# Kernel tuning notes

Measured on AMD Instinct MI355X. Metric: run time of the kernel, lower is better.

## Reference

```python
import jax, jax.numpy as jnp
import numpy as np

TEMPERATURE = 8.0  # sqrt(d_k=64)
NEG = -1e15


def setup_inputs() -> dict:
    key = jax.random.key(0)
    k1, k2, k3, k4, k5 = jax.random.split(key, 5)
    BH, L, D = 64, 1024, 64  # B=4 examples x H=16 heads
    B = 4
    q = jax.random.normal(k1, (BH, L, D), dtype=jnp.float32)
    k = jax.random.normal(k2, (BH, L, D), dtype=jnp.float32)
    v = jax.random.normal(k3, (BH, L, D), dtype=jnp.float32)
    mask = jax.random.randint(k4, (BH, L, L), 0, 2).astype(jnp.bool_)
    edge = jax.random.randint(k5, (B, L, L), 0, 2).astype(jnp.int32)
    return {"q": q, "k": k, "v": v, "mask": mask, "edge": edge}


def reference(q, k, v, mask, edge):
    # attn = q @ k^T / temperature : [BH, L, L]
    attn = jnp.einsum('bld,bmd->blm', q, k) / TEMPERATURE
    # edge.repeat(BH // B, 1, 1): torch repeat == tile along batch dim
    rep = attn.shape[0] // edge.shape[0]
    edge_t = jnp.tile(edge, (rep, 1, 1))
    attn = jnp.where(edge_t == 0, NEG, attn)
    attn = jnp.where(mask, NEG, attn)
    attn = jax.nn.softmax(attn, axis=2)
    # dropout p=0 -> identity
    output = jnp.einsum('blm,bmd->bld', attn, v)
    return (output, attn)
```

## Files before the change

kernel.cpp:

```cpp
#include <hip/hip_runtime.h>
#include <hip/hip_bf16.h>

#define L_ 1024
#define BH_ 64
#define NEGV (-1e15f)
#define QSCALE 0.18033688011112043f

typedef float f32x4 __attribute__((ext_vector_type(4)));
typedef short s16x8 __attribute__((ext_vector_type(8)));
typedef unsigned short ushort_t;

__device__ __forceinline__ unsigned short f2bf(float f) {
    return __builtin_bit_cast(unsigned short, __float2bfloat16(f));
}
__device__ __forceinline__ unsigned selw(uint4 v, int i) {
    switch (i) { case 0: return v.x; case 1: return v.y; case 2: return v.z; default: return v.w; }
}
__device__ __forceinline__ unsigned spread4(unsigned n) {
    return (n & 1u) | ((n & 2u) << 3) | ((n & 4u) << 6) | ((n & 8u) << 9);
}
__device__ __forceinline__ unsigned pack_bytes_nz(uint4 m) {
    unsigned u = 0;
    #pragma unroll
    for (int k = 0; k < 4; ++k) {
        const unsigned x = selw(m, k);
        u |= ((x & 0x000000FFu) ? 1u : 0u) << (k * 4 + 0);
        u |= ((x & 0x0000FF00u) ? 1u : 0u) << (k * 4 + 1);
        u |= ((x & 0x00FF0000u) ? 1u : 0u) << (k * 4 + 2);
        u |= ((x & 0xFF000000u) ? 1u : 0u) << (k * 4 + 3);
    }
    return u;
}

template<bool TESTZERO>
__device__ __forceinline__ unsigned row_bits_i32(uint4 e0, uint4 e1, uint4 e2, uint4 e3, int ln)
{
    #define BAL_(v) (TESTZERO ? __ballot((v) == 0u) : __ballot((v) != 0u))
    const unsigned long long b00 = BAL_(e0.x), b01 = BAL_(e0.y), b02 = BAL_(e0.z), b03 = BAL_(e0.w);
    const unsigned long long b10 = BAL_(e1.x), b11 = BAL_(e1.y), b12 = BAL_(e1.z), b13 = BAL_(e1.w);
    const unsigned long long b20 = BAL_(e2.x), b21 = BAL_(e2.y), b22 = BAL_(e2.z), b23 = BAL_(e2.w);
    const unsigned long long b30 = BAL_(e3.x), b31 = BAL_(e3.y), b32 = BAL_(e3.z), b33 = BAL_(e3.w);
    #undef BAL_
    const int q0 = ln >> 4, sh = (ln & 15) << 2;
    unsigned u = 0;
    unsigned long long bp;
    bp = q0 == 0 ? b00 : q0 == 1 ? b10 : q0 == 2 ? b20 : b30;
    u |= spread4((unsigned)((bp >> sh) & 0xF)) << 0;
    bp = q0 == 0 ? b01 : q0 == 1 ? b11 : q0 == 2 ? b21 : b31;
    u |= spread4((unsigned)((bp >> sh) & 0xF)) << 1;
    bp = q0 == 0 ? b02 : q0 == 1 ? b12 : q0 == 2 ? b22 : b32;
    u |= spread4((unsigned)((bp >> sh) & 0xF)) << 2;
    bp = q0 == 0 ? b03 : q0 == 1 ? b13 : q0 == 2 ? b23 : b33;
    u |= spread4((unsigned)((bp >> sh) & 0xF)) << 3;
    return u;
}

__global__ __launch_bounds__(256)
void prep1(const int* __restrict__ edgep, ushort_t* __restrict__ mb)
{
    const int wv = threadIdx.x >> 6, ln = threadIdx.x & 63;
    #pragma unroll
    for (int it = 0; it < 4; ++it) {
        const int r   = (blockIdx.x << 4) + (it << 2) + wv;
        const int eb  = r >> 10, row = r & 1023;
        const int rb  = ((eb << 10) + row) << 10;
        const uint4 e0 = *((const uint4*)(edgep + rb) + ln);
        const uint4 e1 = *((const uint4*)(edgep + rb + 256) + ln);
        const uint4 e2 = *((const uint4*)(edgep + rb + 512) + ln);
        const uint4 e3 = *((const uint4*)(edgep + rb + 768) + ln);
        const unsigned u = row_bits_i32<true>(e0, e1, e2, e3, ln);
        const int pp = ((ln & 7) << 3) + (ln >> 3);
        #pragma unroll
        for (int bq = 0; bq < 16; ++bq) {
            const int bh = (bq << 2) + eb;
            mb[((size_t)((bh << 10) + row) << 6) + pp] = (ushort_t)u;
        }
    }
}

__global__ __launch_bounds__(256)
void prep2(const float* __restrict__ vp, const unsigned char* __restrict__ maskp,
           ushort_t* __restrict__ mb, ushort_t* __restrict__ vt)
{
    __shared__ float tile[64][68];
    const int b = blockIdx.x;
    if (b < 2048) {
        const int wv = threadIdx.x >> 6, ln = threadIdx.x & 63;
        unsigned det = 0;
        const unsigned* mu = (const unsigned*)maskp;
        #pragma unroll
        for (int i = 0; i < 16; ++i) det |= mu[i];
        const bool mask_i32 = ((det & 0xFFFFFF00u) == 0u);
        #pragma unroll
        for (int it = 0; it < 8; ++it) {
            const int r = (b << 5) + (it << 2) + wv;
            unsigned u;
            if (!mask_i32) {
                const uint4 m = *((const uint4*)(maskp + ((size_t)r << 10)) + ln);
                u = pack_bytes_nz(m);
            } else {
                const int* mp = (const int*)maskp + ((size_t)r << 10);
                const uint4 m0 = *((const uint4*)mp + ln);
                const uint4 m1 = *((const uint4*)(mp + 256) + ln);
                const uint4 m2 = *((const uint4*)(mp + 512) + ln);
                const uint4 m3 = *((const uint4*)(mp + 768) + ln);
                u = row_bits_i32<false>(m0, m1, m2, m3, ln);
            }
            const int pp = ((ln & 7) << 3) + (ln >> 3);
            mb[((size_t)r << 6) + pp] |= (ushort_t)u;
        }
    } else {
        const int idx = b - 2048;
        const int bh = idx >> 2, kq = (idx & 3) << 8;
        const int t = threadIdx.x;
        for (int ks = 0; ks < 4; ++ks) {
            const int k0 = kq + (ks << 6);
            {
                const int kr = t >> 2, d0 = (t & 3) << 4;
                const float* src = vp + ((size_t)(((bh << 10) + k0 + kr)) << 6) + d0;
                const float4 v0 = *(const float4*)(src);
                const float4 v1 = *(const float4*)(src + 4);
                const float4 v2 = *(const float4*)(src + 8);
                const float4 v3 = *(const float4*)(src + 12);
                *(float4*)&tile[kr][d0]      = v0;
                *(float4*)&tile[kr][d0 + 4]  = v1;
                *(float4*)&tile[kr][d0 + 8]  = v2;
                *(float4*)&tile[kr][d0 + 12] = v3;
            }
            __syncthreads();
            {
                const int d = t >> 2, kc = (t & 3) << 4;
                unsigned uu[8];
                #pragma unroll
                for (int j = 0; j < 16; ++j) {
                    const unsigned short h = f2bf(tile[kc + j][d]);
                    if (j & 1) uu[j >> 1] |= ((unsigned)h) << 16;
                    else       uu[j >> 1] = (unsigned)h;
                }
                ushort_t* dst = vt + ((size_t)((bh << 6) + d) << 10) + k0 + kc;
                *(uint4*)(dst)     = (uint4){uu[0], uu[1], uu[2], uu[3]};
                *(uint4*)(dst + 8) = (uint4){uu[4], uu[5], uu[6], uu[7]};
            }
            __syncthreads();
        }
    }
}

__device__ __forceinline__ void kwrite(ushort_t* stg, int tid, float4 r0, float4 r1, float4 r2, float4 r3)
{
    s16x8 w0, w1;
    w0[0] = (short)f2bf(r0.x); w0[1] = (short)f2bf(r0.y);
    w0[2] = (short)f2bf(r0.z); w0[3] = (short)f2bf(r0.w);
    w0[4] = (short)f2bf(r1.x); w0[5] = (short)f2bf(r1.y);
    w0[6] = (short)f2bf(r1.z); w0[7] = (short)f2bf(r1.w);
    w1[0] = (short)f2bf(r2.x); w1[1] = (short)f2bf(r2.y);
    w1[2] = (short)f2bf(r2.z); w1[3] = (short)f2bf(r2.w);
    w1[4] = (short)f2bf(r3.x); w1[5] = (short)f2bf(r3.y);
    w1[6] = (short)f2bf(r3.z); w1[7] = (short)f2bf(r3.w);
    char* base = (char*)stg + ((tid >> 2) << 7);
    const int sw = (tid >> 2) & 7;
    const int j0 = (tid & 3) << 1;
    *(s16x8*)(base + ((j0 ^ sw) << 4)) = w0;
    *(s16x8*)(base + (((j0 + 1) ^ sw) << 4)) = w1;
}

template<int USE_WS>
__global__ __launch_bounds__(512, 6)
void attn_main(const float* __restrict__ qp, const float* __restrict__ kp,
               const float* __restrict__ vp, const unsigned char* __restrict__ maskp,
               const int* __restrict__ edgep, float* __restrict__ outO,
               float* __restrict__ outA, const ushort_t* __restrict__ vtp,
               const ushort_t* __restrict__ mbp)
{
    __shared__ __align__(16) ushort_t p_lds[16 * 1024];
    __shared__ __align__(16) ushort_t stage[8192];
    __shared__ __align__(16) ushort_t q_lds[1024];
    __shared__ float part[16][8];
    __shared__ float gred[16];

    const int tid  = threadIdx.x;
    const int lane = tid & 63;
    const int w    = tid >> 6;
    const int g    = lane >> 4;
    const int ln   = lane & 15;

    const int bid  = blockIdx.x;
    const int xcd  = bid & 7;
    const int slot = bid >> 3;
    const int bh   = xcd + ((slot >> 6) << 3);
    const int r0   = (slot & 63) << 4;

    bool mask_i32 = false;
    if (!USE_WS) {
        unsigned det = 0;
        const unsigned* mu = (const unsigned*)maskp;
        #pragma unroll
        for (int i = 0; i < 16; ++i) det |= mu[i];
        mask_i32 = ((det & 0xFFFFFF00u) == 0u);
    }

    uint4 br[4];
    if (USE_WS) {
        const ushort_t* mrow = mbp + ((size_t)(((bh << 10) + r0 + (g << 2))) << 6) + (w << 3);
        br[0] = *(const uint4*)(mrow);
        br[1] = *(const uint4*)(mrow + 64);
        br[2] = *(const uint4*)(mrow + 128);
        br[3] = *(const uint4*)(mrow + 192);
    }

    float4 k00, k01, k02, k03;
    {
        const float4* src = (const float4*)(kp + ((size_t)(bh << 10) << 6)) + (tid << 2);
        k00 = src[0]; k01 = src[1]; k02 = src[2]; k03 = src[3];
    }
    if (tid < 256) {
        const float4 qv = *((const float4*)(qp + ((size_t)((bh << 10) + r0) << 6)) + tid);
        const unsigned lo = (unsigned)f2bf(qv.x * QSCALE) | ((unsigned)f2bf(qv.y * QSCALE) << 16);
        const unsigned hi = (unsigned)f2bf(qv.z * QSCALE) | ((unsigned)f2bf(qv.w * QSCALE) << 16);
        const int qrow = tid >> 4, qch = (tid & 15) >> 1;
        char* qd = (char*)q_lds + (qrow << 7) + (((qch ^ (qrow & 7))) << 4) + ((tid & 1) << 3);
        uint2 u2; u2.x = lo; u2.y = hi;
        *(uint2*)qd = u2;
    }
    kwrite(stage, tid, k00, k01, k02, k03);
    __syncthreads();

    const int swp = ln & 7;
    const s16x8 a0 = *(const s16x8*)((char*)q_lds + (ln << 7) + ((g ^ swp) << 4));
    const s16x8 a1 = *(const s16x8*)((char*)q_lds + (ln << 7) + (((4 + g) ^ swp) << 4));

    float rs[4] = {0.f, 0.f, 0.f, 0.f};

    #pragma unroll
    for (int kt = 0; kt < 8; ++kt) {
        float4 nx0, nx1, nx2, nx3;
        uint4 vx0, vx1;
        if (kt < 7) {
            const float4* src = (const float4*)(kp + ((size_t)(((bh << 10) + ((kt + 1) << 7))) << 6)) + (tid << 2);
            nx0 = src[0]; nx1 = src[1]; nx2 = src[2]; nx3 = src[3];
        } else if (USE_WS) {
            const uint4* vs = (const uint4*)(vtp + ((size_t)((bh << 6) + (tid >> 3)) << 10) + ((tid & 7) << 4));
            vx0 = vs[0]; vx1 = vs[1];
        }

        const char* kb = (const char*)stage + (((w << 4) + ln) << 7);
        const s16x8 b0 = *(const s16x8*)(kb + ((g ^ swp) << 4));
        const s16x8 b1 = *(const s16x8*)(kb + (((4 + g) ^ swp) << 4));
        f32x4 acc = {0.f, 0.f, 0.f, 0.f};
        acc = __builtin_amdgcn_mfma_f32_16x16x32_bf16(a0, b0, acc, 0, 0, 0);
        acc = __builtin_amdgcn_mfma_f32_16x16x32_bf16(a1, b1, acc, 0, 0, 0);

        #pragma unroll
        for (int reg = 0; reg < 4; ++reg) {
            float sv = acc[reg];
            if (USE_WS) {
                const unsigned mw = selw(br[reg], kt >> 1);
                if ((mw >> (((kt & 1) << 4) + ln)) & 1u) sv = NEGV;
            } else {
                const int row = r0 + (g << 2) + reg;
                const int col = (kt << 7) + (w << 4) + ln;
                int mv;
                if (mask_i32) mv = ((const int*)maskp)[((size_t)((bh << 10) + row) << 10) + col];
                else          mv = (int)maskp[((size_t)((bh << 10) + row) << 10) + col];
                if (edgep[((size_t)((((bh & 3) << 10) + row)) << 10) + col] == 0 || mv != 0) sv = NEGV;
            }
            const float e = __builtin_amdgcn_exp2f(sv);
            rs[reg] += e;
            const int prow = (g << 2) + reg;
            char* pd = (char*)p_lds + (prow << 11)
                     + ((((kt << 4) + (w << 1) + (ln >> 3)) ^ (prow & 7)) << 4) + ((ln & 7) << 1);
            *(ushort_t*)pd = f2bf(e);
        }
        __syncthreads();
        if (kt < 7) {
            kwrite(stage, tid, nx0, nx1, nx2, nx3);
        } else if (USE_WS) {
            char* bse = (char*)stage + ((tid >> 3) << 8);
            const int sw2 = (tid >> 3) & 7;
            const int ch0 = (tid & 7) << 1;
            *(uint4*)(bse + ((ch0 ^ sw2) << 4)) = vx0;
            *(uint4*)(bse + (((ch0 + 1) ^ sw2) << 4)) = vx1;
        }
        __syncthreads();
    }

    #pragma unroll
    for (int reg = 0; reg < 4; ++reg) {
        float s = rs[reg];
        s += __shfl_xor(s, 1);
        s += __shfl_xor(s, 2);
        s += __shfl_xor(s, 4);
        s += __shfl_xor(s, 8);
        if (ln == 0) part[(g << 2) + reg][w] = s;
    }
    __syncthreads();
    if (tid < 16) {
        float s = part[tid][0];
        #pragma unroll
        for (int i = 1; i < 8; ++i) s += part[tid][i];
        gred[tid] = __builtin_amdgcn_rcpf(s);
    }
    __syncthreads();

    const int dt = w & 3, kh = w >> 2;
    f32x4 acco = {0.f, 0.f, 0.f, 0.f};
    #pragma unroll
    for (int kt = 0; kt < 8; ++kt) {
        uint4 vx0, vx1;
        if (USE_WS && kt < 7) {
            const uint4* vs = (const uint4*)(vtp + ((size_t)((bh << 6) + (tid >> 3)) << 10)
                                             + ((kt + 1) << 7) + ((tid & 7) << 4));
            vx0 = vs[0]; vx1 = vs[1];
        }
        const char* pl = (const char*)p_lds + (ln << 11);
        const s16x8 pa0 = *(const s16x8*)(pl + ((((kt << 4) + (kh << 3) + g) ^ swp) << 4));
        const s16x8 pa1 = *(const s16x8*)(pl + ((((kt << 4) + (kh << 3) + 4 + g) ^ swp) << 4));
        s16x8 vbf0, vbf1;
        if (USE_WS) {
            const char* vb = (const char*)stage + (((dt << 4) + ln) << 8);
            vbf0 = *(const s16x8*)(vb + ((((kh << 3) + g) ^ swp) << 4));
            vbf1 = *(const s16x8*)(vb + ((((kh << 3) + 4 + g) ^ swp) << 4));
        } else {
            #pragma unroll
            for (int j = 0; j < 8; ++j) {
                const int k1 = (kt << 7) + (kh << 6) + (g << 3) + j;
                vbf0[j] = (short)f2bf(vp[((size_t)((bh << 10) + k1) << 6) + (dt << 4) + ln]);
                vbf1[j] = (short)f2bf(vp[((size_t)((bh << 10) + k1 + 32) << 6) + (dt << 4) + ln]);
            }
        }
        acco = __builtin_amdgcn_mfma_f32_16x16x32_bf16(pa0, vbf0, acco, 0, 0, 0);
        acco = __builtin_amdgcn_mfma_f32_16x16x32_bf16(pa1, vbf1, acco, 0, 0, 0);
        __syncthreads();
        if (USE_WS && kt < 7) {
            char* bse = (char*)stage + ((tid >> 3) << 8);
            const int sw2 = (tid >> 3) & 7;
            const int ch0 = (tid & 7) << 1;
            *(uint4*)(bse + ((ch0 ^ sw2) << 4)) = vx0;
            *(uint4*)(bse + (((ch0 + 1) ^ sw2) << 4)) = vx1;
        }
        __syncthreads();
    }

    float* op = (float*)stage;
    if (kh == 1) {
        #pragma unroll
        for (int reg = 0; reg < 4; ++reg)
            op[((dt << 4) + (g << 2) + reg) * 17 + ln] = acco[reg];
    }
    __syncthreads();
    if (kh == 0) {
        #pragma unroll
        for (int reg = 0; reg < 4; ++reg) {
            const int rl = (g << 2) + reg;
            const float v = (acco[reg] + op[((dt << 4) + rl) * 17 + ln]) * gred[rl];
            outO[((size_t)((bh << 10) + r0 + rl) << 6) + (dt << 4) + ln] = v;
        }
    }

    {
        const char* src = (const char*)p_lds;
        float* dstf = outA + ((size_t)((bh << 10) + r0) << 10);
        #pragma unroll
        for (int i = 0; i < 4; ++i) {
            const unsigned boff = (unsigned)((i * 512 + tid) << 4);
            const int rl = (int)(boff >> 11);
            const float rinv = gred[rl];
            const uint4 d4 = *(const uint4*)(src + (boff ^ ((rl & 7) << 4)));
            float4 f0, f1;
            f0.x = __builtin_bit_cast(float, d4.x << 16) * rinv;
            f0.y = __builtin_bit_cast(float, d4.x & 0xFFFF0000u) * rinv;
            f0.z = __builtin_bit_cast(float, d4.y << 16) * rinv;
            f0.w = __builtin_bit_cast(float, d4.y & 0xFFFF0000u) * rinv;
            f1.x = __builtin_bit_cast(float, d4.z << 16) * rinv;
            f1.y = __builtin_bit_cast(float, d4.z & 0xFFFF0000u) * rinv;
            f1.z = __builtin_bit_cast(float, d4.w << 16) * rinv;
            f1.w = __builtin_bit_cast(float, d4.w & 0xFFFF0000u) * rinv;
            char* db = (char*)dstf + ((size_t)boff << 1);
            *(float4*)db = f0;
            *(float4*)(db + 16) = f1;
        }
    }
}

extern "C" void kernel_launch(void* const* d_in, const int* in_sizes, int n_in,
                              void* d_out, int out_size, void* d_ws, size_t ws_size,
                              hipStream_t stream)
{
    (void)in_sizes; (void)n_in; (void)out_size;
    const float* qp = (const float*)d_in[0];
    const float* kp = (const float*)d_in[1];
    const float* vp = (const float*)d_in[2];
    const unsigned char* maskp = (const unsigned char*)d_in[3];
    const int* edgep = (const int*)d_in[4];

    float* outO = (float*)d_out;
    float* outA = outO + ((long long)BH_ * L_ * 64);

    const size_t vt_bytes = (size_t)BH_ * 64 * L_ * 2;
    const size_t mb_bytes = (size_t)BH_ * L_ * 64 * 2;
    const int use_ws = (d_ws != nullptr && ws_size >= vt_bytes + mb_bytes) ? 1 : 0;

    ushort_t* vt = (ushort_t*)d_ws;
    ushort_t* mb = (ushort_t*)((char*)d_ws + vt_bytes);

    if (use_ws) {
        prep1<<<256, 256, 0, stream>>>(edgep, mb);
        prep2<<<2304, 256, 0, stream>>>(vp, maskp, mb, vt);
        attn_main<1><<<4096, 512, 0, stream>>>(qp, kp, vp, maskp, edgep, outO, outA, vt, mb);
    } else {
        attn_main<0><<<4096, 512, 0, stream>>>(qp, kp, vp, maskp, edgep, outO, outA, vt, mb);
    }
}
```

Before: 246.2 us.

## Pre-convert Q/K/V to swizzled bf16 and double-buffer K/V tiles with async LDS loads

```diff
diff --git a/kernel.cpp b/kernel.cpp
--- a/kernel.cpp
+++ b/kernel.cpp
@@ -30,6 +30,11 @@
         u |= ((x & 0xFF000000u) ? 1u : 0u) << (k * 4 + 3);
     }
     return u;
+}
+__device__ __forceinline__ void gl_lds16(const void* g, void* l) {
+    __builtin_amdgcn_global_load_lds(
+        (const __attribute__((address_space(1))) unsigned int*)g,
+        (__attribute__((address_space(3))) unsigned int*)l, 16, 0, 0);
 }
 
 template<bool TESTZERO>
@@ -56,196 +61,179 @@
 }
 
 __global__ __launch_bounds__(256)
-void prep1(const int* __restrict__ edgep, ushort_t* __restrict__ mb)
+void prep(const float* __restrict__ qp, const float* __restrict__ kp,
+          const float* __restrict__ vp, const unsigned char* __restrict__ maskp,
+          const int* __restrict__ edgep, ushort_t* __restrict__ ws)
 {
-    const int wv = threadIdx.x >> 6, ln = threadIdx.x & 63;
-    #pragma unroll
-    for (int it = 0; it < 4; ++it) {
-        const int r   = (blockIdx.x << 4) + (it << 2) + wv;
-        const int eb  = r >> 10, row = r & 1023;
-        const int rb  = ((eb << 10) + row) << 10;
-        const uint4 e0 = *((const uint4*)(edgep + rb) + ln);
-        const uint4 e1 = *((const uint4*)(edgep + rb + 256) + ln);
-        const uint4 e2 = *((const uint4*)(edgep + rb + 512) + ln);
-        const uint4 e3 = *((const uint4*)(edgep + rb + 768) + ln);
-        const unsigned u = row_bits_i32<true>(e0, e1, e2, e3, ln);
+    __shared__ float tile[128][68];
+    ushort_t* Kp = ws;
+    ushort_t* Vp = ws + (1u << 22);
+    ushort_t* Qp = ws + (2u << 22);
+    ushort_t* Mp = ws + (3u << 22);
+
+    const int b = blockIdx.x;
+    const int t = threadIdx.x;
+
+    if (b < 1024) {
+        const int wv = t >> 6, ln = t & 63;
+        const int rid = (b << 2) + wv;
+        const int eb = rid >> 10, row = rid & 1023;
+
+        unsigned det = 0;
+        const unsigned* mu = (const unsigned*)maskp;
+        #pragma unroll
+        for (int i = 0; i < 16; ++i) det |= mu[i];
+        const bool mask_i32 = ((det & 0xFFFFFF00u) == 0u);
+
+        unsigned ewv;
+        {
+            const int rb = ((eb << 10) + row) << 10;
+            const uint4 e0 = *((const uint4*)(edgep + rb) + ln);
+            const uint4 e1 = *((const uint4*)(edgep + rb + 256) + ln);
+            const uint4 e2 = *((const uint4*)(edgep + rb + 512) + ln);
+            const uint4 e3 = *((const uint4*)(edgep + rb + 768) + ln);
+            ewv = row_bits_i32<true>(e0, e1, e2, e3, ln);
+        }
         const int pp = ((ln & 7) << 3) + (ln >> 3);
-        #pragma unroll
         for (int bq = 0; bq < 16; ++bq) {
             const int bh = (bq << 2) + eb;
-            mb[((size_t)((bh << 10) + row) << 6) + pp] = (ushort_t)u;
-        }
-    }
-}
-
-__global__ __launch_bounds__(256)
-void prep2(const float* __restrict__ vp, const unsigned char* __restrict__ maskp,
-           ushort_t* __restrict__ mb, ushort_t* __restrict__ vt)
-{
-    __shared__ float tile[64][68];
-    const int b = blockIdx.x;
-    if (b < 2048) {
-        const int wv = threadIdx.x >> 6, ln = threadIdx.x & 63;
-        unsigned det = 0;
-        const unsigned* mu = (const unsigned*)maskp;
-        #pragma unroll
-        for (int i = 0; i < 16; ++i) det |= mu[i];
-        const bool mask_i32 = ((det & 0xFFFFFF00u) == 0u);
-        #pragma unroll
-        for (int it = 0; it < 8; ++it) {
-            const int r = (b << 5) + (it << 2) + wv;
-            unsigned u;
+            unsigned u = ewv;
             if (!mask_i32) {
-                const uint4 m = *((const uint4*)(maskp + ((size_t)r << 10)) + ln);
-                u = pack_bytes_nz(m);
+                const uint4 m = *((const uint4*)(maskp + ((size_t)((bh << 10) + row) << 10)) + ln);
+                u |= pack_bytes_nz(m);
             } else {
-                const int* mp = (const int*)maskp + ((size_t)r << 10);
+                const int* mp = (const int*)maskp + ((size_t)((bh << 10) + row) << 10);
                 const uint4 m0 = *((const uint4*)mp + ln);
                 const uint4 m1 = *((const uint4*)(mp + 256) + ln);
                 const uint4 m2 = *((const uint4*)(mp + 512) + ln);
                 const uint4 m3 = *((const uint4*)(mp + 768) + ln);
-                u = row_bits_i32<false>(m0, m1, m2, m3, ln);
+                u |= row_bits_i32<false>(m0, m1, m2, m3, ln);
             }
-            const int pp = ((ln & 7) << 3) + (ln >> 3);
-            mb[((size_t)r << 6) + pp] |= (ushort_t)u;
+            Mp[((size_t)((bh << 10) + row) << 6) + pp] = (ushort_t)u;
+        }
+    } else if (b < 1536) {
+        const int idx = b - 1024;
+        const int bh = idx >> 3, vt = idx & 7;
+        const float* vsrc = vp + (((size_t)(bh << 10) + (vt << 7)) << 6);
+        #pragma unroll
+        for (int i = 0; i < 8; ++i) {
+            const int f4 = (i << 8) + t;
+            const int k = f4 >> 4, d4 = f4 & 15;
+            *(float4*)&tile[k][d4 << 2] = *((const float4*)vsrc + f4);
+        }
+        __syncthreads();
+        ushort_t* dst = Vp + ((size_t)((bh << 3) + vt) << 13);
+        #pragma unroll
+        for (int i = 0; i < 4; ++i) {
+            const int ci = (t << 2) + i;
+            const int d = ci >> 4, p = ci & 15;
+            const int c = p ^ (d & 7);
+            s16x8 o;
+            #pragma unroll
+            for (int j = 0; j < 8; ++j) o[j] = (short)f2bf(tile[(c << 3) + j][d]);
+            *(s16x8*)(dst + (ci << 3)) = o;
+        }
+    } else if (b < 2048) {
+        const int idx = b - 1536;
+        const int bh = idx >> 3, kt = idx & 7;
+        const int r = t >> 1, h = t & 1;
+        const float* src = kp + (((size_t)((bh << 10) + (kt << 7) + r)) << 6) + (h << 5);
+        float v[32];
+        #pragma unroll
+        for (int j = 0; j < 8; ++j) *(float4*)&v[j << 2] = *((const float4*)src + j);
+        ushort_t* dst = Kp + ((size_t)((bh << 3) + kt) << 13) + (r << 6);
+        #pragma unroll
+        for (int q = 0; q < 4; ++q) {
+            const int c = (h << 2) + q;
+            const int s = c ^ (r & 7);
+            s16x8 o;
+            #pragma unroll
+            for (int j = 0; j < 8; ++j) o[j] = (short)f2bf(v[(q << 3) + j]);
+            *(s16x8*)(dst + (s << 3)) = o;
         }
     } else {
-        const int idx = b - 2048;
-        const int bh = idx >> 2, kq = (idx & 3) << 8;
-        const int t = threadIdx.x;
-        for (int ks = 0; ks < 4; ++ks) {
-            const int k0 = kq + (ks << 6);
-            {
-                const int kr = t >> 2, d0 = (t & 3) << 4;
-                const float* src = vp + ((size_t)(((bh << 10) + k0 + kr)) << 6) + d0;
-                const float4 v0 = *(const float4*)(src);
-                const float4 v1 = *(const float4*)(src + 4);
-                const float4 v2 = *(const float4*)(src + 8);
-                const float4 v3 = *(const float4*)(src + 12);
-                *(float4*)&tile[kr][d0]      = v0;
-                *(float4*)&tile[kr][d0 + 4]  = v1;
-                *(float4*)&tile[kr][d0 + 8]  = v2;
-                *(float4*)&tile[kr][d0 + 12] = v3;
-            }
-            __syncthreads();
-            {
-                const int d = t >> 2, kc = (t & 3) << 4;
-                unsigned uu[8];
-                #pragma unroll
-                for (int j = 0; j < 16; ++j) {
-                    const unsigned short h = f2bf(tile[kc + j][d]);
-                    if (j & 1) uu[j >> 1] |= ((unsigned)h) << 16;
-                    else       uu[j >> 1] = (unsigned)h;
-                }
-                ushort_t* dst = vt + ((size_t)((bh << 6) + d) << 10) + k0 + kc;
-                *(uint4*)(dst)     = (uint4){uu[0], uu[1], uu[2], uu[3]};
-                *(uint4*)(dst + 8) = (uint4){uu[4], uu[5], uu[6], uu[7]};
-            }
-            __syncthreads();
-        }
-    }
-}
-
-__device__ __forceinline__ void kwrite(ushort_t* stg, int tid, float4 r0, float4 r1, float4 r2, float4 r3)
-{
-    s16x8 w0, w1;
-    w0[0] = (short)f2bf(r0.x); w0[1] = (short)f2bf(r0.y);
-    w0[2] = (short)f2bf(r0.z); w0[3] = (short)f2bf(r0.w);
-    w0[4] = (short)f2bf(r1.x); w0[5] = (short)f2bf(r1.y);
-    w0[6] = (short)f2bf(r1.z); w0[7] = (short)f2bf(r1.w);
-    w1[0] = (short)f2bf(r2.x); w1[1] = (short)f2bf(r2.y);
-    w1[2] = (short)f2bf(r2.z); w1[3] = (short)f2bf(r2.w);
-    w1[4] = (short)f2bf(r3.x); w1[5] = (short)f2bf(r3.y);
-    w1[6] = (short)f2bf(r3.z); w1[7] = (short)f2bf(r3.w);
-    char* base = (char*)stg + ((tid >> 2) << 7);
-    const int sw = (tid >> 2) & 7;
-    const int j0 = (tid & 3) << 1;
-    *(s16x8*)(base + ((j0 ^ sw) << 4)) = w0;
-    *(s16x8*)(base + (((j0 + 1) ^ sw) << 4)) = w1;
-}
-
-template<int USE_WS>
-__global__ __launch_bounds__(512, 6)
-void attn_main(const float* __restrict__ qp, const float* __restrict__ kp,
-               const float* __restrict__ vp, const unsigned char* __restrict__ maskp,
-               const int* __restrict__ edgep, float* __restrict__ outO,
-               float* __restrict__ outA, const ushort_t* __restrict__ vtp,
-               const ushort_t* __restrict__ mbp)
+        const int bh = b - 2048;
+        const int wv = t >> 6, ln = t & 63;
+        for (int i = 0; i < 16; ++i) {
+            const int rt = (i << 2) + wv;
+            const int r = (rt << 4) + (ln & 15), gq = ln >> 4;
+            const float* src = qp + (((size_t)((bh << 10) + r)) << 6) + (gq << 3);
+            const float4 q0 = *(const float4*)src;
+            const float4 q1 = *(const float4*)(src + 4);
+            const float4 q2 = *(const float4*)(src + 32);
+            const float4 q3 = *(const float4*)(src + 36);
+            s16x8 a, bfr;
+            a[0]=(short)f2bf(q0.x*QSCALE); a[1]=(short)f2bf(q0.y*QSCALE);
+            a[2]=(short)f2bf(q0.z*QSCALE); a[3]=(short)f2bf(q0.w*QSCALE);
+            a[4]=(short)f2bf(q1.x*QSCALE); a[5]=(short)f2bf(q1.y*QSCALE);
+            a[6]=(short)f2bf(q1.z*QSCALE); a[7]=(short)f2bf(q1.w*QSCALE);
+            bfr[0]=(short)f2bf(q2.x*QSCALE); bfr[1]=(short)f2bf(q2.y*QSCALE);
+            bfr[2]=(short)f2bf(q2.z*QSCALE); bfr[3]=(short)f2bf(q2.w*QSCALE);
+            bfr[4]=(short)f2bf(q3.x*QSCALE); bfr[5]=(short)f2bf(q3.y*QSCALE);
+            bfr[6]=(short)f2bf(q3.z*QSCALE); bfr[7]=(short)f2bf(q3.w*QSCALE);
+            ushort_t* dst = Qp + ((size_t)((bh << 6) + rt) << 10) + (ln << 4);
+            *(s16x8*)(dst) = a;
+            *(s16x8*)(dst + 8) = bfr;
+        }
+    }
+}
+
+__global__ __launch_bounds__(512, 4)
+void attn_main(const ushort_t* __restrict__ ws, float* __restrict__ outO,
+               float* __restrict__ outA)
 {
     __shared__ __align__(16) ushort_t p_lds[16 * 1024];
-    __shared__ __align__(16) ushort_t stage[8192];
-    __shared__ __align__(16) ushort_t q_lds[1024];
+    __shared__ __align__(16) ushort_t stage[2][8192];
     __shared__ float part[16][8];
     __shared__ float gred[16];
 
-    const int tid  = threadIdx.x;
-    const int lane = tid & 63;
-    const int w    = tid >> 6;
-    const int g    = lane >> 4;
-    const int ln   = lane & 15;
-
-    const int bid  = blockIdx.x;
-    const int xcd  = bid & 7;
-    const int slot = bid >> 3;
-    const int bh   = xcd + ((slot >> 6) << 3);
-    const int r0   = (slot & 63) << 4;
-
-    bool mask_i32 = false;
-    if (!USE_WS) {
-        unsigned det = 0;
-        const unsigned* mu = (const unsigned*)maskp;
-        #pragma unroll
-        for (int i = 0; i < 16; ++i) det |= mu[i];
-        mask_i32 = ((det & 0xFFFFFF00u) == 0u);
-    }
+    const ushort_t* Kp = ws;
+    const ushort_t* Vp = ws + (1u << 22);
+    const ushort_t* Qp = ws + (2u << 22);
+    const ushort_t* Mp = ws + (3u << 22);
+
+    const int tid = threadIdx.x, lane = tid & 63, w = tid >> 6;
+    const int g = lane >> 4, ln = lane & 15;
+    const int bid = blockIdx.x, xcd = bid & 7, slot = bid >> 3;
+    const int bh = xcd + ((slot >> 6) << 3);
+    const int rt = slot & 63;
+    const int r0 = rt << 4;
+    const int sb = w << 1;
+
+    const ushort_t* qs = Qp + ((size_t)((bh << 6) + rt) << 10) + (lane << 4);
+    const s16x8 a0 = *(const s16x8*)(qs);
+    const s16x8 a1 = *(const s16x8*)(qs + 8);
 
     uint4 br[4];
-    if (USE_WS) {
-        const ushort_t* mrow = mbp + ((size_t)(((bh << 10) + r0 + (g << 2))) << 6) + (w << 3);
+    {
+        const ushort_t* mrow = Mp + ((size_t)((bh << 10) + r0 + (g << 2)) << 6) + (w << 3);
         br[0] = *(const uint4*)(mrow);
         br[1] = *(const uint4*)(mrow + 64);
         br[2] = *(const uint4*)(mrow + 128);
         br[3] = *(const uint4*)(mrow + 192);
     }
 
-    float4 k00, k01, k02, k03;
-    {
-        const float4* src = (const float4*)(kp + ((size_t)(bh << 10) << 6)) + (tid << 2);
-        k00 = src[0]; k01 = src[1]; k02 = src[2]; k03 = src[3];
-    }
-    if (tid < 256) {
-        const float4 qv = *((const float4*)(qp + ((size_t)((bh << 10) + r0) << 6)) + tid);
-        const unsigned lo = (unsigned)f2bf(qv.x * QSCALE) | ((unsigned)f2bf(qv.y * QSCALE) << 16);
-        const unsigned hi = (unsigned)f2bf(qv.z * QSCALE) | ((unsigned)f2bf(qv.w * QSCALE) << 16);
-        const int qrow = tid >> 4, qch = (tid & 15) >> 1;
-        char* qd = (char*)q_lds + (qrow << 7) + (((qch ^ (qrow & 7))) << 4) + ((tid & 1) << 3);
-        uint2 u2; u2.x = lo; u2.y = hi;
-        *(uint2*)qd = u2;
-    }
-    kwrite(stage, tid, k00, k01, k02, k03);
-    __syncthreads();
-
-    const int swp = ln & 7;
-    const s16x8 a0 = *(const s16x8*)((char*)q_lds + (ln << 7) + ((g ^ swp) << 4));
-    const s16x8 a1 = *(const s16x8*)((char*)q_lds + (ln << 7) + (((4 + g) ^ swp) << 4));
+    #define STAGE_(base, tt, cc)                                                   \
+        gl_lds16(base + ((size_t)(bh) << 16) + ((tt) << 13) + ((sb + 0) << 9) + (lane << 3), \
+                 &stage[cc][(sb + 0) << 9]);                                       \
+        gl_lds16(base + ((size_t)(bh) << 16) + ((tt) << 13) + ((sb + 1) << 9) + (lane << 3), \
+                 &stage[cc][(sb + 1) << 9]);
+
+    STAGE_(Kp, 0, 0);
+    __syncthreads();
 
     float rs[4] = {0.f, 0.f, 0.f, 0.f};
 
     #pragma unroll
     for (int kt = 0; kt < 8; ++kt) {
-        float4 nx0, nx1, nx2, nx3;
-        uint4 vx0, vx1;
-        if (kt < 7) {
-            const float4* src = (const float4*)(kp + ((size_t)(((bh << 10) + ((kt + 1) << 7))) << 6)) + (tid << 2);
-            nx0 = src[0]; nx1 = src[1]; nx2 = src[2]; nx3 = src[3];
-        } else if (USE_WS) {
-            const uint4* vs = (const uint4*)(vtp + ((size_t)((bh << 6) + (tid >> 3)) << 10) + ((tid & 7) << 4));
-            vx0 = vs[0]; vx1 = vs[1];
-        }
-
-        const char* kb = (const char*)stage + (((w << 4) + ln) << 7);
-        const s16x8 b0 = *(const s16x8*)(kb + ((g ^ swp) << 4));
-        const s16x8 b1 = *(const s16x8*)(kb + (((4 + g) ^ swp) << 4));
+        const int cur = kt & 1, nxt = cur ^ 1;
+        if (kt < 7) { STAGE_(Kp, kt + 1, nxt); }
+        else        { STAGE_(Vp, 0, nxt); }
+
+        const int rw = (w << 4) + ln;
+        const char* kb = (const char*)stage[cur] + (rw << 7);
+        const s16x8 b0 = *(const s16x8*)(kb + (((g)     ^ (rw & 7)) << 4));
+        const s16x8 b1 = *(const s16x8*)(kb + (((4 + g) ^ (rw & 7)) << 4));
         f32x4 acc = {0.f, 0.f, 0.f, 0.f};
         acc = __builtin_amdgcn_mfma_f32_16x16x32_bf16(a0, b0, acc, 0, 0, 0);
         acc = __builtin_amdgcn_mfma_f32_16x16x32_bf16(a1, b1, acc, 0, 0, 0);
@@ -253,33 +241,15 @@
         #pragma unroll
         for (int reg = 0; reg < 4; ++reg) {
             float sv = acc[reg];
-            if (USE_WS) {
-                const unsigned mw = selw(br[reg], kt >> 1);
-                if ((mw >> (((kt & 1) << 4) + ln)) & 1u) sv = NEGV;
-            } else {
-                const int row = r0 + (g << 2) + reg;
-                const int col = (kt << 7) + (w << 4) + ln;
-                int mv;
-                if (mask_i32) mv = ((const int*)maskp)[((size_t)((bh << 10) + row) << 10) + col];
-                else          mv = (int)maskp[((size_t)((bh << 10) + row) << 10) + col];
-                if (edgep[((size_t)((((bh & 3) << 10) + row)) << 10) + col] == 0 || mv != 0) sv = NEGV;
-            }
+            const unsigned mw = selw(br[reg], kt >> 1);
+            if ((mw >> (((kt & 1) << 4) + ln)) & 1u) sv = NEGV;
             const float e = __builtin_amdgcn_exp2f(sv);
             rs[reg] += e;
             const int prow = (g << 2) + reg;
             char* pd = (char*)p_lds + (prow << 11)
-                     + ((((kt << 4) + (w << 1) + (ln >> 3)) ^ (prow & 7)) << 4) + ((ln & 7) << 1);
+                     + ((((kt << 4) + (w << 1) + (ln >> 3)) ^ (prow & 7)) << 4)
+                     + ((ln & 7) << 1);
             *(ushort_t*)pd = f2bf(e);
-        }
-        __syncthreads();
-        if (kt < 7) {
-            kwrite(stage, tid, nx0, nx1, nx2, nx3);
-        } else if (USE_WS) {
-            char* bse = (char*)stage + ((tid >> 3) << 8);
-            const int sw2 = (tid >> 3) & 7;
-            const int ch0 = (tid & 7) << 1;
-            *(uint4*)(bse + ((ch0 ^ sw2) << 4)) = vx0;
-            *(uint4*)(bse + (((ch0 + 1) ^ sw2) << 4)) = vx1;
         }
         __syncthreads();
     }
@@ -305,43 +275,23 @@
     const int dt = w & 3, kh = w >> 2;
     f32x4 acco = {0.f, 0.f, 0.f, 0.f};
     #pragma unroll
-    for (int kt = 0; kt < 8; ++kt) {
-        uint4 vx0, vx1;
-        if (USE_WS && kt < 7) {
-            const uint4* vs = (const uint4*)(vtp + ((size_t)((bh << 6) + (tid >> 3)) << 10)
-                                             + ((kt + 1) << 7) + ((tid & 7) << 4));
-            vx0 = vs[0]; vx1 = vs[1];
-        }
+    for (int ut = 0; ut < 8; ++ut) {
+        const int cur = ut & 1, nxt = cur ^ 1;
+        if (ut < 7) { STAGE_(Vp, ut + 1, nxt); }
+
         const char* pl = (const char*)p_lds + (ln << 11);
-        const s16x8 pa0 = *(const s16x8*)(pl + ((((kt << 4) + (kh << 3) + g) ^ swp) << 4));
-        const s16x8 pa1 = *(const s16x8*)(pl + ((((kt << 4) + (kh << 3) + 4 + g) ^ swp) << 4));
-        s16x8 vbf0, vbf1;
-        if (USE_WS) {
-            const char* vb = (const char*)stage + (((dt << 4) + ln) << 8);
-            vbf0 = *(const s16x8*)(vb + ((((kh << 3) + g) ^ swp) << 4));
-            vbf1 = *(const s16x8*)(vb + ((((kh << 3) + 4 + g) ^ swp) << 4));
-        } else {
-            #pragma unroll
-            for (int j = 0; j < 8; ++j) {
-                const int k1 = (kt << 7) + (kh << 6) + (g << 3) + j;
-                vbf0[j] = (short)f2bf(vp[((size_t)((bh << 10) + k1) << 6) + (dt << 4) + ln]);
-                vbf1[j] = (short)f2bf(vp[((size_t)((bh << 10) + k1 + 32) << 6) + (dt << 4) + ln]);
-            }
-        }
-        acco = __builtin_amdgcn_mfma_f32_16x16x32_bf16(pa0, vbf0, acco, 0, 0, 0);
-        acco = __builtin_amdgcn_mfma_f32_16x16x32_bf16(pa1, vbf1, acco, 0, 0, 0);
+        const s16x8 pa0 = *(const s16x8*)(pl + ((((ut << 4) + (kh << 3) + g)     ^ (ln & 7)) << 4));
+        const s16x8 pa1 = *(const s16x8*)(pl + ((((ut << 4) + (kh << 3) + 4 + g) ^ (ln & 7)) << 4));
+        const char* vb = (const char*)stage[cur] + (((dt << 4) + ln) << 8);
+        const s16x8 vb0 = *(const s16x8*)(vb + ((((kh << 3) + g)     ^ (ln & 7)) << 4));
+        const s16x8 vb1 = *(const s16x8*)(vb + ((((kh << 3) + 4 + g) ^ (ln & 7)) << 4));
+        acco = __builtin_amdgcn_mfma_f32_16x16x32_bf16(pa0, vb0, acco, 0, 0, 0);
+        acco = __builtin_amdgcn_mfma_f32_16x16x32_bf16(pa1, vb1, acco, 0, 0, 0);
         __syncthreads();
-        if (USE_WS && kt < 7) {
-            char* bse = (char*)stage + ((tid >> 3) << 8);
-            const int sw2 = (tid >> 3) & 7;
-            const int ch0 = (tid & 7) << 1;
-            *(uint4*)(bse + ((ch0 ^ sw2) << 4)) = vx0;
-            *(uint4*)(bse + (((ch0 + 1) ^ sw2) << 4)) = vx1;
-        }
-        __syncthreads();
-    }
-
-    float* op = (float*)stage;
+    }
+    #undef STAGE_
+
+    float* op = (float*)&stage[0][0];
     if (kh == 1) {
         #pragma unroll
         for (int reg = 0; reg < 4; ++reg)
@@ -352,8 +302,8 @@
         #pragma unroll
         for (int reg = 0; reg < 4; ++reg) {
             const int rl = (g << 2) + reg;
-            const float v = (acco[reg] + op[((dt << 4) + rl) * 17 + ln]) * gred[rl];
-            outO[((size_t)((bh << 10) + r0 + rl) << 6) + (dt << 4) + ln] = v;
+            outO[((size_t)((bh << 10) + r0 + rl) << 6) + (dt << 4) + ln] =
+                (acco[reg] + op[((dt << 4) + rl) * 17 + ln]) * gred[rl];
         }
     }
 
@@ -382,6 +332,142 @@
     }
 }
 
+__global__ __launch_bounds__(512)
+void attn_fb(const float* __restrict__ qp, const float* __restrict__ kp,
+             const float* __restrict__ vp, const unsigned char* __restrict__ maskp,
+             const int* __restrict__ edgep, float* __restrict__ outO,
+             float* __restrict__ outA)
+{
+    __shared__ __align__(16) ushort_t p_lds[16 * 1024];
+    __shared__ float part[16][8];
+    __shared__ float gred[16];
+    __shared__ float opart[4][16][17];
+
+    const int tid = threadIdx.x, lane = tid & 63, w = tid >> 6;
+    const int g = lane >> 4, ln = lane & 15;
+    const int bid = blockIdx.x, xcd = bid & 7, slot = bid >> 3;
+    const int bh = xcd + ((slot >> 6) << 3);
+    const int r0 = (slot & 63) << 4;
+    const int c0 = w << 7;
+
+    unsigned det = 0;
+    const unsigned* mu = (const unsigned*)maskp;
+    #pragma unroll
+    for (int i = 0; i < 16; ++i) det |= mu[i];
+    const bool mask_i32 = ((det & 0xFFFFFF00u) == 0u);
+
+    const float* qb = qp + (((size_t)((bh << 10) + r0 + ln)) << 6) + (g << 3);
+    s16x8 a0, a1;
+    #pragma unroll
+    for (int j = 0; j < 8; ++j) {
+        a0[j] = (short)f2bf(qb[j] * QSCALE);
+        a1[j] = (short)f2bf(qb[j + 32] * QSCALE);
+    }
+
+    f32x4 acc[8];
+    #pragma unroll
+    for (int nt = 0; nt < 8; ++nt) acc[nt] = (f32x4){0.f, 0.f, 0.f, 0.f};
+    #pragma unroll
+    for (int nt = 0; nt < 8; ++nt) {
+        const float* kb = kp + (((size_t)((bh << 10) + c0 + (nt << 4) + ln)) << 6) + (g << 3);
+        s16x8 b0, b1;
+        #pragma unroll
+        for (int j = 0; j < 8; ++j) {
+            b0[j] = (short)f2bf(kb[j]);
+            b1[j] = (short)f2bf(kb[j + 32]);
+        }
+        acc[nt] = __builtin_amdgcn_mfma_f32_16x16x32_bf16(a0, b0, acc[nt], 0, 0, 0);
+        acc[nt] = __builtin_amdgcn_mfma_f32_16x16x32_bf16(a1, b1, acc[nt], 0, 0, 0);
+    }
+
+    float rs[4] = {0.f, 0.f, 0.f, 0.f};
+    #pragma unroll
+    for (int reg = 0; reg < 4; ++reg) {
+        const int row = r0 + (g << 2) + reg;
+        #pragma unroll
+        for (int nt = 0; nt < 8; ++nt) {
+            const int col = c0 + (nt << 4) + ln;
+            float sv = acc[nt][reg];
+            int mv;
+            if (mask_i32) mv = ((const int*)maskp)[((size_t)((bh << 10) + row) << 10) + col];
+            else          mv = (int)maskp[((size_t)((bh << 10) + row) << 10) + col];
+            if (edgep[((size_t)((((bh & 3) << 10) + row)) << 10) + col] == 0 || mv != 0) sv = NEGV;
+            const float e = __builtin_amdgcn_exp2f(sv);
+            rs[reg] += e;
+            const int rl = (g << 2) + reg;
+            const unsigned off = ((unsigned)((rl << 11) | (col << 1))) ^ ((rl & 7) << 4);
+            *(ushort_t*)((char*)p_lds + off) = f2bf(e);
+        }
+    }
+    #pragma unroll
+    for (int reg = 0; reg < 4; ++reg) {
+        float s = rs[reg];
+        s += __shfl_xor(s, 1);
+        s += __shfl_xor(s, 2);
+        s += __shfl_xor(s, 4);
+        s += __shfl_xor(s, 8);
+        if (ln == 0) part[(g << 2) + reg][w] = s;
+    }
+    __syncthreads();
+    if (tid < 16) {
+        float s = part[tid][0];
+        #pragma unroll
+        for (int i = 1; i < 8; ++i) s += part[tid][i];
+        gred[tid] = __builtin_amdgcn_rcpf(s);
+    }
+    __syncthreads();
+
+    const int dt = w & 3, kh = w >> 2;
+    f32x4 acco = {0.f, 0.f, 0.f, 0.f};
+    for (int kt = 0; kt < 16; ++kt) {
+        const int ktg = (kh << 4) + kt;
+        const unsigned offA = ((unsigned)((ln << 11) | (ktg << 6) | (g << 4))) ^ ((ln & 7) << 4);
+        const s16x8 pa = *(const s16x8*)((const char*)p_lds + offA);
+        s16x8 vb;
+        #pragma unroll
+        for (int j = 0; j < 8; ++j)
+            vb[j] = (short)f2bf(vp[((size_t)((bh << 10) + (ktg << 5) + (g << 3) + j) << 6) + (dt << 4) + ln]);
+        acco = __builtin_amdgcn_mfma_f32_16x16x32_bf16(pa, vb, acco, 0, 0, 0);
+    }
+    if (kh == 1) {
+        #pragma unroll
+        for (int reg = 0; reg < 4; ++reg)
+            opart[dt][(g << 2) + reg][ln] = acco[reg];
+    }
+    __syncthreads();
+    if (kh == 0) {
+        #pragma unroll
+        for (int reg = 0; reg < 4; ++reg) {
+            const int rl = (g << 2) + reg;
+            outO[((size_t)((bh << 10) + r0 + rl) << 6) + (dt << 4) + ln] =
+                (acco[reg] + opart[dt][rl][ln]) * gred[rl];
+        }
+    }
+    {
+        const char* src = (const char*)p_lds;
+        float* dstf = outA + ((size_t)((bh << 10) + r0) << 10);
+        #pragma unroll
+        for (int i = 0; i < 4; ++i) {
+            const unsigned boff = (unsigned)((i * 512 + tid) << 4);
+            const int rl = (int)(boff >> 11);
+            const float rinv = gred[rl];
+            const uint4 d4 = *(const uint4*)(src + (boff ^ ((rl & 7) << 4)));
+            float4 f0, f1;
+            f0.x = __builtin_bit_cast(float, d4.x << 16) * rinv;
+            f0.y = __builtin_bit_cast(float, d4.x & 0xFFFF0000u) * rinv;
+            f0.z = __builtin_bit_cast(float, d4.y << 16) * rinv;
+            f0.w = __builtin_bit_cast(float, d4.y & 0xFFFF0000u) * rinv;
+            f1.x = __builtin_bit_cast(float, d4.z << 16) * rinv;
+            f1.y = __builtin_bit_cast(float, d4.z & 0xFFFF0000u) * rinv;
+            f1.z = __builtin_bit_cast(float, d4.w << 16) * rinv;
+            f1.w = __builtin_bit_cast(float, d4.w & 0xFFFF0000u) * rinv;
+            char* db = (char*)dstf + ((size_t)boff << 1);
+            *(float4*)db = f0;
+            *(float4*)(db + 16) = f1;
+        }
+    }
+}
+
 extern "C" void kernel_launch(void* const* d_in, const int* in_sizes, int n_in,
                               void* d_out, int out_size, void* d_ws, size_t ws_size,
                               hipStream_t stream)
@@ -396,18 +482,12 @@
     float* outO = (float*)d_out;
     float* outA = outO + ((long long)BH_ * L_ * 64);
 
-    const size_t vt_bytes = (size_t)BH_ * 64 * L_ * 2;
-    const size_t mb_bytes = (size_t)BH_ * L_ * 64 * 2;
-    const int use_ws = (d_ws != nullptr && ws_size >= vt_bytes + mb_bytes) ? 1 : 0;
-
-    ushort_t* vt = (ushort_t*)d_ws;
-    ushort_t* mb = (ushort_t*)((char*)d_ws + vt_bytes);
-
-    if (use_ws) {
-        prep1<<<256, 256, 0, stream>>>(edgep, mb);
-        prep2<<<2304, 256, 0, stream>>>(vp, maskp, mb, vt);
-        attn_main<1><<<4096, 512, 0, stream>>>(qp, kp, vp, maskp, edgep, outO, outA, vt, mb);
+    const size_t need = (size_t)32 * 1024 * 1024;
+    if (d_ws != nullptr && ws_size >= need) {
+        ushort_t* ws = (ushort_t*)d_ws;
+        prep<<<2112, 256, 0, stream>>>(qp, kp, vp, maskp, edgep, ws);
+        attn_main<<<4096, 512, 0, stream>>>(ws, outO, outA);
     } else {
-        attn_main<0><<<4096, 512, 0, stream>>>(qp, kp, vp, maskp, edgep, outO, outA, vt, mb);
-    }
-}
+        attn_fb<<<4096, 512, 0, stream>>>(qp, kp, vp, maskp, edgep, outO, outA);
+    }
+}
```

New measurement: 239.5 us. 2.7% less time.
